# Optimization experiments

Hardware: AMD Instinct MI355X
Metric: run time of the kernel (lower is better)

## Reference

```python
import jax, jax.numpy as jnp
import numpy as np

N_NODES = 50000
N_EDGES = 800000
IN_DIM = 128
EDGE_DIM = 32
HID = 64


def _glorot(key, shape):
    fan_in, fan_out = shape[0], shape[1]
    lim = float(np.sqrt(6.0 / (fan_in + fan_out)))
    return jax.random.uniform(key, shape, jnp.float32, -lim, lim)


def setup_inputs() -> dict:
    key = jax.random.key(0)
    ks = jax.random.split(key, 16)
    x = jax.random.normal(ks[0], (N_NODES, IN_DIM), jnp.float32)
    edge_index = jax.random.randint(ks[1], (2, N_EDGES), 0, N_NODES, jnp.int64)
    edge_attr = jax.random.normal(ks[2], (N_EDGES, EDGE_DIM), jnp.float32)
    message = jax.random.normal(ks[3], (N_EDGES, HID), jnp.float32)
    return {
        "x": x,
        "edge_index": edge_index,
        "edge_attr": edge_attr,
        "message": message,
        "W_src": _glorot(ks[4], (IN_DIM, HID)),
        "W_dest": _glorot(ks[5], (IN_DIM, HID)),
        "W_edge": _glorot(ks[6], (EDGE_DIM, HID)),
        "attn_vec": _glorot(ks[7], (1, HID)),
        "mlp_w1": _glorot(ks[8], (2 * HID, HID)),
        "mlp_b1": jnp.zeros((HID,), jnp.float32),
        "bn1_g": jnp.ones((HID,), jnp.float32),
        "bn1_b": jnp.zeros((HID,), jnp.float32),
        "mlp_w2": _glorot(ks[9], (HID, HID)),
        "mlp_b2": jnp.zeros((HID,), jnp.float32),
        "bn2_g": jnp.ones((HID,), jnp.float32),
        "bn2_b": jnp.zeros((HID,), jnp.float32),
        "amlp_w": _glorot(ks[10], (HID, 1)),
        "amlp_b": jnp.zeros((1,), jnp.float32),
    }


def _batchnorm(h, g, b, eps=1e-5):
    mu = jnp.mean(h, axis=0)
    var = jnp.var(h, axis=0)  # biased, as torch BN training forward
    return (h - mu) * jax.lax.rsqrt(var + eps) * g + b


def _segment_softmax(scores, seg, num_segments):
    m = jax.ops.segment_max(scores, seg, num_segments=num_segments)
    m = jnp.where(jnp.isneginf(m), 0.0, m)
    e = jnp.exp(scores - m[seg])
    s = jax.ops.segment_sum(e, seg, num_segments=num_segments)
    return e / s[seg]


def _scatter_max0(vals, seg, num_segments):
    # torch_scatter reduce='max' fills empty segments with 0
    out = jax.ops.segment_max(vals, seg, num_segments=num_segments)
    return jnp.where(jnp.isneginf(out), 0.0, out)


def reference(x, edge_index, edge_attr, message, W_src, W_dest, W_edge, attn_vec,
              mlp_w1, mlp_b1, bn1_g, bn1_b, mlp_w2, mlp_b2, bn2_g, bn2_b,
              amlp_w, amlp_b):
    row, col = edge_index[0], edge_index[1]
    # attention scores per edge
    h = x[row] @ W_src + x[col] @ W_dest + edge_attr @ W_edge  # [E, H]
    scores = jax.nn.leaky_relu(h @ attn_vec[0], negative_slope=0.2)  # [E]
    attn = _segment_softmax(scores, col, N_NODES)  # [E]
    msg = message * attn[:, None]  # [E, H]
    fwd = _scatter_max0(msg, col, N_NODES)  # [N, H]
    bwd = _scatter_max0(msg, row, N_NODES)  # [N, H]
    out = jnp.concatenate([fwd, bwd], axis=1)  # [N, 2H]
    # node MLP (BatchNorm in training-stats mode, dropout disabled)
    h1 = jax.nn.relu(_batchnorm(out @ mlp_w1 + mlp_b1, bn1_g, bn1_b))
    h2 = jax.nn.relu(_batchnorm(h1 @ mlp_w2 + mlp_b2, bn2_g, bn2_b))
    gate = jax.nn.sigmoid(h2 @ amlp_w + amlp_b).reshape(-1)  # [N]
    return h2, gate
```

## Files before the change

### kernel.cpp

```cpp
#include <hip/hip_runtime.h>
#include <hip/hip_bf16.h>
#include <float.h>

#define IN_DIM 128
#define EDGE_DIM 32
#define HID 64
#define BKT_G 64
#define BCAP 3072
#define NBKT_MAX 784
#define CHUNK 4096

__global__ void k_uvw(const float* __restrict__ Wsrc, const float* __restrict__ Wdst,
                      const float* __restrict__ Wedge, const float* __restrict__ avec,
                      const int* __restrict__ ei32, int* sflag,
                      float* u, float* v, float* w) {
    if (blockIdx.x == 0 && threadIdx.x == 0) {
        int odd_or = ei32[1] | ei32[3] | ei32[5] | ei32[7] | ei32[9] | ei32[11];
        sflag[0] = (odd_or == 0) ? 2 : 1;
    }
    int wave = (blockIdx.x * blockDim.x + threadIdx.x) >> 6;
    int lane = threadIdx.x & 63;
    const float* src; float* dst; int row;
    if (wave < 128)      { src = Wsrc;  dst = u; row = wave; }
    else if (wave < 256) { src = Wdst;  dst = v; row = wave - 128; }
    else if (wave < 288) { src = Wedge; dst = w; row = wave - 256; }
    else return;
    float acc = src[row * HID + lane] * avec[lane];
    for (int o = 32; o >= 1; o >>= 1) acc += __shfl_xor(acc, o);
    if (lane == 0) dst[row] = acc;
}

__global__ void k_pq(const float* __restrict__ x, const float* __restrict__ u,
                     const float* __restrict__ v, float* p, float* q, int N) {
    int wave = (blockIdx.x * blockDim.x + threadIdx.x) >> 6;
    int lane = threadIdx.x & 63;
    if (wave >= N) return;
    const float* xr = x + (size_t)wave * IN_DIM;
    float a0 = xr[lane], a1 = xr[lane + 64];
    float pp = a0 * u[lane] + a1 * u[lane + 64];
    float qq = a0 * v[lane] + a1 * v[lane + 64];
    for (int m = 32; m >= 1; m >>= 1) { pp += __shfl_xor(pp, m); qq += __shfl_xor(qq, m); }
    if (lane == 0) { p[wave] = pp; q[wave] = qq; }
}

__global__ void k_edot(const float* __restrict__ ea, const float* __restrict__ w,
                       float* rdot, int E) {
    int gid = blockIdx.x * blockDim.x + threadIdx.x;
    int e = gid >> 3;
    int j = gid & 7;
    if (e >= E) return;
    float4 av = ((const float4*)ea)[(size_t)e * 8 + j];
    float4 wv = ((const float4*)w)[j];
    float val = av.x * wv.x + av.y * wv.y + av.z * wv.z + av.w * wv.w;
    val += __shfl_xor(val, 4);
    val += __shfl_xor(val, 2);
    val += __shfl_xor(val, 1);
    if (j == 0) rdot[e] = val;
}

__global__ __launch_bounds__(256) void k_binscore(const int* __restrict__ ei,
                                                  const int* __restrict__ sflag,
                                                  const float* __restrict__ rdot,
                                                  const float* __restrict__ p,
                                                  const float* __restrict__ q,
                                                  float* scores,
                                                  int* gcur_col, int* gcur_row,
                                                  unsigned* bbuf_col, unsigned* bbuf_row,
                                                  int E, int nbkt) {
    __shared__ int lc[NBKT_MAX], lrw[NBKT_MAX];
    __shared__ int gc[NBKT_MAX], grw[NBKT_MAX];
    int tid = threadIdx.x;
    int e0 = blockIdx.x * CHUNK;
    int e1 = e0 + CHUNK; if (e1 > E) e1 = E;
    for (int i = tid; i < nbkt; i += 256) { lc[i] = 0; lrw[i] = 0; }
    __syncthreads();
    int st = sflag[0];
    for (int e = e0 + tid; e < e1; e += 256) {
        int r = ei[(size_t)st * e];
        int c = ei[(size_t)st * (E + e)];
        float sc = rdot[e] + p[r] + q[c];
        scores[e] = (sc > 0.f) ? sc : 0.2f * sc;
        atomicAdd(&lc[c >> 6], 1);
        atomicAdd(&lrw[r >> 6], 1);
    }
    __syncthreads();
    for (int b = tid; b < nbkt; b += 256) {
        int n1 = lc[b];  if (n1) gc[b]  = atomicAdd(&gcur_col[b], n1);
        int n2 = lrw[b]; if (n2) grw[b] = atomicAdd(&gcur_row[b], n2);
        lc[b] = 0; lrw[b] = 0;
    }
    __syncthreads();
    for (int e = e0 + tid; e < e1; e += 256) {
        int r = ei[(size_t)st * e];
        int c = ei[(size_t)st * (E + e)];
        int pos = gc[c >> 6] + atomicAdd(&lc[c >> 6], 1);
        if (pos < BCAP) bbuf_col[(size_t)(c >> 6) * BCAP + pos] = (unsigned)((e << 6) | (c & 63));
        int pos2 = grw[r >> 6] + atomicAdd(&lrw[r >> 6], 1);
        if (pos2 < BCAP) bbuf_row[(size_t)(r >> 6) * BCAP + pos2] = (unsigned)((e << 6) | (r & 63));
    }
}

__global__ __launch_bounds__(512) void k_sortfwd(float* scores, const float* __restrict__ msg,
                                                 const int* __restrict__ bcur,
                                                 const unsigned* __restrict__ bbuf,
                                                 float* fwd, int N) {
    __shared__ unsigned raw[BCAP];
    __shared__ unsigned srt[BCAP];
    __shared__ float    ssc[BCAP];
    __shared__ int cnt[BKT_G], cur[BKT_G], sstart[BKT_G + 1];
    int b = blockIdx.x, tid = threadIdx.x;
    int M = bcur[b]; if (M > BCAP) M = BCAP;
    if (tid < BKT_G) cnt[tid] = 0;
    __syncthreads();
    for (int i = tid; i < M; i += 512) {
        unsigned v = bbuf[(size_t)b * BCAP + i];
        raw[i] = v;
        atomicAdd(&cnt[v & 63], 1);
    }
    __syncthreads();
    if (tid < BKT_G) {
        int val = cnt[tid];
        int inc = val;
        for (int off = 1; off < BKT_G; off <<= 1) {
            int o = __shfl_up(inc, off);
            if (tid >= off) inc += o;
        }
        sstart[tid + 1] = inc;
        if (tid == 0) sstart[0] = 0;
        cur[tid] = inc - val;
    }
    __syncthreads();
    for (int j = tid; j < M; j += 512) {
        unsigned v = raw[j];
        int posn = atomicAdd(&cur[v & 63], 1);
        srt[posn] = v;
    }
    __syncthreads();
    for (int i = tid; i < M; i += 512) ssc[i] = scores[srt[i] >> 6];
    __syncthreads();
    int wave = tid >> 6, lane = tid & 63;
    for (int n = wave; n < BKT_G; n += 8) {
        int node = b * BKT_G + n;
        if (node >= N) continue;
        int a0 = sstart[n], len = sstart[n + 1] - a0;
        if (len == 0) { fwd[(size_t)node * HID + lane] = 0.f; continue; }
        float m = -FLT_MAX;
        for (int k = lane; k < len; k += 64) m = fmaxf(m, ssc[a0 + k]);
        for (int o = 32; o >= 1; o >>= 1) m = fmaxf(m, __shfl_xor(m, o));
        float ssum = 0.f;
        for (int k = lane; k < len; k += 64) ssum += expf(ssc[a0 + k] - m);
        for (int o = 32; o >= 1; o >>= 1) ssum += __shfl_xor(ssum, o);
        float rcp = 1.f / ssum;
        for (int k = lane; k < len; k += 64) {
            int i = a0 + k;
            float at = expf(ssc[i] - m) * rcp;
            ssc[i] = at;
            scores[srt[i] >> 6] = at;
        }
        asm volatile("s_waitcnt lgkmcnt(0)" ::: "memory");
        float acc = -FLT_MAX;
        int k = 0;
        for (; k + 8 <= len; k += 8) {
            float vv[8];
#pragma unroll
            for (int u8 = 0; u8 < 8; u8++) {
                int i = a0 + k + u8;
                vv[u8] = msg[(size_t)(srt[i] >> 6) * HID + lane] * ssc[i];
            }
#pragma unroll
            for (int u8 = 0; u8 < 8; u8++) acc = fmaxf(acc, vv[u8]);
        }
        for (; k < len; k++) {
            int i = a0 + k;
            acc = fmaxf(acc, msg[(size_t)(srt[i] >> 6) * HID + lane] * ssc[i]);
        }
        fwd[(size_t)node * HID + lane] = acc;
    }
}

__global__ __launch_bounds__(512) void k_sortbwd(const float* __restrict__ scores,
                                                 const float* __restrict__ msg,
                                                 const int* __restrict__ bcur,
                                                 const unsigned* __restrict__ bbuf,
                                                 float* bwd, int N) {
    __shared__ unsigned raw[BCAP];
    __shared__ unsigned srt[BCAP];
    __shared__ float    ssc[BCAP];
    __shared__ int cnt[BKT_G], cur[BKT_G], sstart[BKT_G + 1];
    int b = blockIdx.x, tid = threadIdx.x;
    int M = bcur[b]; if (M > BCAP) M = BCAP;
    if (tid < BKT_G) cnt[tid] = 0;
    __syncthreads();
    for (int i = tid; i < M; i += 512) {
        unsigned v = bbuf[(size_t)b * BCAP + i];
        raw[i] = v;
        atomicAdd(&cnt[v & 63], 1);
    }
    __syncthreads();
    if (tid < BKT_G) {
        int val = cnt[tid];
        int inc = val;
        for (int off = 1; off < BKT_G; off <<= 1) {
            int o = __shfl_up(inc, off);
            if (tid >= off) inc += o;
        }
        sstart[tid + 1] = inc;
        if (tid == 0) sstart[0] = 0;
        cur[tid] = inc - val;
    }
    __syncthreads();
    for (int j = tid; j < M; j += 512) {
        unsigned v = raw[j];
        int posn = atomicAdd(&cur[v & 63], 1);
        srt[posn] = v;
    }
    __syncthreads();
    for (int i = tid; i < M; i += 512) ssc[i] = scores[srt[i] >> 6];
    __syncthreads();
    int wave = tid >> 6, lane = tid & 63;
    for (int n = wave; n < BKT_G; n += 8) {
        int node = b * BKT_G + n;
        if (node >= N) continue;
        int a0 = sstart[n], len = sstart[n + 1] - a0;
        if (len == 0) { bwd[(size_t)node * HID + lane] = 0.f; continue; }
        float acc = -FLT_MAX;
        int k = 0;
        for (; k + 8 <= len; k += 8) {
            float vv[8];
#pragma unroll
            for (int u8 = 0; u8 < 8; u8++) {
                int i = a0 + k + u8;
                vv[u8] = msg[(size_t)(srt[i] >> 6) * HID + lane] * ssc[i];
            }
#pragma unroll
            for (int u8 = 0; u8 < 8; u8++) acc = fmaxf(acc, vv[u8]);
        }
        for (; k < len; k++) {
            int i = a0 + k;
            acc = fmaxf(acc, msg[(size_t)(srt[i] >> 6) * HID + lane] * ssc[i]);
        }
        bwd[(size_t)node * HID + lane] = acc;
    }
}

__global__ __launch_bounds__(256) void k_mlp1(const float* __restrict__ fwd,
                                              const float* __restrict__ bwd,
                                              const float* __restrict__ W1,
                                              const float* __restrict__ b1,
                                              float* pre1, float* gsum, float* gss, int N) {
    __shared__ float lsum[HID], lss[HID];
    int t = threadIdx.x;
    if (t < HID) { lsum[t] = 0.f; lss[t] = 0.f; }
    __syncthreads();
    int h = t & 63, lr = t >> 6;
    float bh = b1[h];
    float s = 0.f, ssq = 0.f;
    for (int n = blockIdx.x * 4 + lr; n < N; n += gridDim.x * 4) {
        const float* fr = fwd + (size_t)n * HID;
        const float* br = bwd + (size_t)n * HID;
        float acc = bh;
        for (int k = 0; k < HID; k++) acc += fr[k] * W1[k * HID + h];
        for (int k = 0; k < HID; k++) acc += br[k] * W1[(HID + k) * HID + h];
        pre1[(size_t)n * HID + h] = acc;
        s += acc; ssq += acc * acc;
    }
    atomicAdd(&lsum[h], s);
    atomicAdd(&lss[h], ssq);
    __syncthreads();
    if (t < HID) { atomicAdd(&gsum[t], lsum[t]); atomicAdd(&gss[t], lss[t]); }
}

__global__ void k_bnfin(const float* __restrict__ gsum, const float* __restrict__ gss,
                        const float* __restrict__ g, const float* __restrict__ b,
                        float* scale, float* shift, int N) {
    int t = threadIdx.x;
    if (t >= HID) return;
    float invN = 1.0f / (float)N;
    float mu = gsum[t] * invN;
    float var = gss[t] * invN - mu * mu;
    float rs = rsqrtf(var + 1e-5f);
    float sc = rs * g[t];
    scale[t] = sc;
    shift[t] = b[t] - mu * sc;
}

__global__ __launch_bounds__(256) void k_mlp2(const float* __restrict__ pre1,
                                              const float* __restrict__ scale1,
                                              const float* __restrict__ shift1,
                                              const float* __restrict__ W2,
                                              const float* __restrict__ b2v,
                                              float* pre2, float* gsum, float* gss, int N) {
    __shared__ float lsum[HID], lss[HID];
    int t = threadIdx.x;
    if (t < HID) { lsum[t] = 0.f; lss[t] = 0.f; }
    __syncthreads();
    int h = t & 63, lr = t >> 6;
    float bh = b2v[h];
    float s = 0.f, ssq = 0.f;
    for (int n = blockIdx.x * 4 + lr; n < N; n += gridDim.x * 4) {
        const float* pr = pre1 + (size_t)n * HID;
        float acc = bh;
        for (int k = 0; k < HID; k++) {
            float z = pr[k] * scale1[k] + shift1[k];
            z = (z > 0.f) ? z : 0.f;
            acc += z * W2[k * HID + h];
        }
        pre2[(size_t)n * HID + h] = acc;
        s += acc; ssq += acc * acc;
    }
    atomicAdd(&lsum[h], s);
    atomicAdd(&lss[h], ssq);
    __syncthreads();
    if (t < HID) { atomicAdd(&gsum[t], lsum[t]); atomicAdd(&gss[t], lss[t]); }
}

__global__ void k_out(const float* __restrict__ pre2, const float* __restrict__ scale2,
                      const float* __restrict__ shift2, const float* __restrict__ amw,
                      const float* __restrict__ amb, float* out, int N) {
    int gid = blockIdx.x * blockDim.x + threadIdx.x;
    int n = gid >> 6, h = gid & 63;
    if (n >= N) return;
    float z = pre2[(size_t)n * HID + h] * scale2[h] + shift2[h];
    float h2 = (z > 0.f) ? z : 0.f;
    out[(size_t)n * HID + h] = h2;
    float part = h2 * amw[h];
    for (int m = 32; m >= 1; m >>= 1) part += __shfl_xor(part, m);
    if (h == 0) {
        float gate = 1.0f / (1.0f + expf(-(part + amb[0])));
        out[(size_t)N * HID + n] = gate;
    }
}

extern "C" void kernel_launch(void* const* d_in, const int* in_sizes, int n_in,
                              void* d_out, int out_size, void* d_ws, size_t ws_size,
                              hipStream_t stream) {
    const float* x     = (const float*)d_in[0];
    const int*   ei    = (const int*)d_in[1];
    const float* ea    = (const float*)d_in[2];
    const float* msg   = (const float*)d_in[3];
    const float* Wsrc  = (const float*)d_in[4];
    const float* Wdst  = (const float*)d_in[5];
    const float* Wedge = (const float*)d_in[6];
    const float* avec  = (const float*)d_in[7];
    const float* W1    = (const float*)d_in[8];
    const float* b1    = (const float*)d_in[9];
    const float* g1    = (const float*)d_in[10];
    const float* bb1   = (const float*)d_in[11];
    const float* W2    = (const float*)d_in[12];
    const float* b2    = (const float*)d_in[13];
    const float* g2    = (const float*)d_in[14];
    const float* bb2   = (const float*)d_in[15];
    const float* amw   = (const float*)d_in[16];
    const float* amb   = (const float*)d_in[17];
    float* out = (float*)d_out;

    const int N = in_sizes[0] / IN_DIM;
    const int E = in_sizes[1] / 2;
    const int NH = N * HID;
    const int nbkt = (N + BKT_G - 1) / BKT_G;

    float* ws = (float*)d_ws;
    float* gsum1  = ws;
    float* gss1   = ws + 64;
    float* gsum2  = ws + 128;
    float* gss2   = ws + 192;
    float* scale1 = ws + 256;
    float* shift1 = ws + 320;
    float* scale2 = ws + 384;
    float* shift2 = ws + 448;
    int*   sflag  = (int*)(ws + 512);
    float* u      = ws + 576;
    float* v      = ws + 704;
    float* w      = ws + 832;
    float* T        = ws + 1024;
    float* p        = T;
    float* q        = p + N;
    float* scores   = q + N;
    float* rdot     = scores + E;
    int*   gcur_col = (int*)(rdot + E);
    int*   gcur_row = gcur_col + nbkt;
    unsigned* bbuf_col = (unsigned*)(gcur_row + nbkt);
    unsigned* bbuf_row = bbuf_col + (size_t)nbkt * BCAP;
    size_t T_words  = 2 * (size_t)N + 2 * (size_t)E + 2 * (size_t)nbkt
                    + 2 * (size_t)nbkt * BCAP;
    size_t T_sz     = (T_words < (size_t)NH) ? (size_t)NH : T_words;
    float* fwd  = ws + 1024 + T_sz;
    float* bwd  = fwd + (size_t)NH;
    float* pre1 = T;
    float* pre2 = fwd;

    (void)hipMemsetAsync(gcur_col, 0, (size_t)2 * nbkt * sizeof(int), stream);
    (void)hipMemsetAsync(ws, 0, 512 * sizeof(float), stream);
    hipLaunchKernelGGL(k_uvw, dim3(72), dim3(256), 0, stream,
                       Wsrc, Wdst, Wedge, avec, ei, sflag, u, v, w);
    hipLaunchKernelGGL(k_pq, dim3((N * 64 + 255) / 256), dim3(256), 0, stream,
                       x, u, v, p, q, N);
    hipLaunchKernelGGL(k_edot, dim3((E * 8 + 255) / 256), dim3(256), 0, stream,
                       ea, w, rdot, E);
    hipLaunchKernelGGL(k_binscore, dim3((E + CHUNK - 1) / CHUNK), dim3(256), 0, stream,
                       ei, sflag, rdot, p, q, scores,
                       gcur_col, gcur_row, bbuf_col, bbuf_row, E, nbkt);
    hipLaunchKernelGGL(k_sortfwd, dim3(nbkt), dim3(512), 0, stream,
                       scores, msg, gcur_col, bbuf_col, fwd, N);
    hipLaunchKernelGGL(k_sortbwd, dim3(nbkt), dim3(512), 0, stream,
                       scores, msg, gcur_row, bbuf_row, bwd, N);
    hipLaunchKernelGGL(k_mlp1, dim3(1024), dim3(256), 0, stream,
                       fwd, bwd, W1, b1, pre1, gsum1, gss1, N);
    hipLaunchKernelGGL(k_bnfin, dim3(1), dim3(64), 0, stream,
                       gsum1, gss1, g1, bb1, scale1, shift1, N);
    hipLaunchKernelGGL(k_mlp2, dim3(1024), dim3(256), 0, stream,
                       pre1, scale1, shift1, W2, b2, pre2, gsum2, gss2, N);
    hipLaunchKernelGGL(k_bnfin, dim3(1), dim3(64), 0, stream,
                       gsum2, gss2, g2, bb2, scale2, shift2, N);
    hipLaunchKernelGGL(k_out, dim3((N * 64 + 255) / 256), dim3(256), 0, stream,
                       pre2, scale2, shift2, amw, amb, out, N);
}
```

Baseline: 372.2 us.

## Fuse node MLP, batchnorm and gate into one cooperative kernel with grid sync

Replaces the five node-MLP launches (mlp1, bnfin, mlp2, bnfin, out) with a single cooperative kernel. Each wave keeps its per-row pre-activations in registers across two grid-wide syncs, and batchnorm statistics are reduced through global atomics. This removes launch overhead and the global round trips for pre1 and pre2. It adds grid.sync cost, depends on all 1024 blocks being co-resident, and falls back to the old launch path if the cooperative launch fails.

```diff
diff --git a/kernel.cpp b/kernel.cpp
--- a/kernel.cpp
+++ b/kernel.cpp
@@ -1,6 +1,9 @@
 #include <hip/hip_runtime.h>
 #include <hip/hip_bf16.h>
+#include <hip/hip_cooperative_groups.h>
 #include <float.h>
+
+namespace cg = cooperative_groups;
 
 #define IN_DIM 128
 #define EDGE_DIM 32
@@ -9,6 +12,8 @@
 #define BCAP 3072
 #define NBKT_MAX 784
 #define CHUNK 4096
+#define MLP_GRID 1024
+#define ROWS_MAX 13
 
 __global__ void k_uvw(const float* __restrict__ Wsrc, const float* __restrict__ Wdst,
                       const float* __restrict__ Wedge, const float* __restrict__ avec,
@@ -243,6 +248,108 @@
     }
 }
 
+__global__ __launch_bounds__(256, 4) void k_mlpfused(
+        const float* __restrict__ fwd, const float* __restrict__ bwd,
+        const float* __restrict__ W1, const float* __restrict__ b1,
+        const float* __restrict__ g1, const float* __restrict__ bb1,
+        const float* __restrict__ W2, const float* __restrict__ b2,
+        const float* __restrict__ g2, const float* __restrict__ bb2,
+        const float* __restrict__ amw, const float* __restrict__ amb,
+        float* gstats, float* out, int N) {
+    cg::grid_group grid = cg::this_grid();
+    __shared__ float lsum[HID], lss[HID];
+    __shared__ float sscale[HID], sshift[HID];
+    const int t = threadIdx.x, h = t & 63, lr = t >> 6;
+    const int nwave = MLP_GRID * 4;
+    const int wgid = blockIdx.x * 4 + lr;
+    float pre1r[ROWS_MAX], pre2r[ROWS_MAX];
+    const float invN = 1.0f / (float)N;
+
+    if (t < HID) { lsum[t] = 0.f; lss[t] = 0.f; }
+    __syncthreads();
+    float bh = b1[h];
+    float s = 0.f, ssq = 0.f;
+#pragma unroll
+    for (int i = 0; i < ROWS_MAX; i++) {
+        int n = wgid + i * nwave;
+        if (n < N) {
+            const float* fr = fwd + (size_t)n * HID;
+            const float* br = bwd + (size_t)n * HID;
+            float acc = bh;
+            for (int k = 0; k < HID; k++) acc += fr[k] * W1[k * HID + h];
+            for (int k = 0; k < HID; k++) acc += br[k] * W1[(HID + k) * HID + h];
+            pre1r[i] = acc;
+            s += acc; ssq += acc * acc;
+        } else pre1r[i] = 0.f;
+    }
+    atomicAdd(&lsum[h], s);
+    atomicAdd(&lss[h], ssq);
+    __syncthreads();
+    if (t < HID) { atomicAdd(&gstats[t], lsum[t]); atomicAdd(&gstats[HID + t], lss[t]); }
+    grid.sync();
+
+    if (t < HID) {
+        float gs = atomicAdd(&gstats[t], 0.0f);
+        float gq = atomicAdd(&gstats[HID + t], 0.0f);
+        float mu = gs * invN;
+        float var = gq * invN - mu * mu;
+        float rs = rsqrtf(var + 1e-5f);
+        float sc = rs * g1[t];
+        sscale[t] = sc;
+        sshift[t] = bb1[t] - mu * sc;
+        lsum[t] = 0.f; lss[t] = 0.f;
+    }
+    __syncthreads();
+
+    float b2h = b2[h];
+    s = 0.f; ssq = 0.f;
+#pragma unroll
+    for (int i = 0; i < ROWS_MAX; i++) {
+        int n = wgid + i * nwave;
+        float z = pre1r[i] * sscale[h] + sshift[h];
+        z = (z > 0.f) ? z : 0.f;
+        float acc = b2h;
+        for (int k = 0; k < HID; k++) {
+            float zk = __shfl(z, k);
+            acc += zk * W2[k * HID + h];
+        }
+        if (n < N) { pre2r[i] = acc; s += acc; ssq += acc * acc; }
+        else pre2r[i] = 0.f;
+    }
+    atomicAdd(&lsum[h], s);
+    atomicAdd(&lss[h], ssq);
+    __syncthreads();
+    if (t < HID) { atomicAdd(&gstats[2 * HID + t], lsum[t]); atomicAdd(&gstats[3 * HID + t], lss[t]); }
+    grid.sync();
+
+    if (t < HID) {
+        float gs = atomicAdd(&gstats[2 * HID + t], 0.0f);
+        float gq = atomicAdd(&gstats[3 * HID + t], 0.0f);
+        float mu = gs * invN;
+        float var = gq * invN - mu * mu;
+        float rs = rsqrtf(var + 1e-5f);
+        float sc = rs * g2[t];
+        sscale[t] = sc;
+        sshift[t] = bb2[t] - mu * sc;
+    }
+    __syncthreads();
+    float aw = amw[h], ab = amb[0];
+#pragma unroll
+    for (int i = 0; i < ROWS_MAX; i++) {
+        int n = wgid + i * nwave;
+        if (n >= N) continue;
+        float z = pre2r[i] * sscale[h] + sshift[h];
+        float h2 = (z > 0.f) ? z : 0.f;
+        out[(size_t)n * HID + h] = h2;
+        float part = h2 * aw;
+        for (int m = 32; m >= 1; m >>= 1) part += __shfl_xor(part, m);
+        if (h == 0) {
+            float gate = 1.0f / (1.0f + expf(-(part + ab)));
+            out[(size_t)N * HID + n] = gate;
+        }
+    }
+}
+
 __global__ __launch_bounds__(256) void k_mlp1(const float* __restrict__ fwd,
                                               const float* __restrict__ bwd,
                                               const float* __restrict__ W1,
@@ -342,16 +449,16 @@
     const float* Wdst  = (const float*)d_in[5];
     const float* Wedge = (const float*)d_in[6];
     const float* avec  = (const float*)d_in[7];
-    const float* W1    = (const float*)d_in[8];
-    const float* b1    = (const float*)d_in[9];
-    const float* g1    = (const float*)d_in[10];
-    const float* bb1   = (const float*)d_in[11];
-    const float* W2    = (const float*)d_in[12];
-    const float* b2    = (const float*)d_in[13];
-    const float* g2    = (const float*)d_in[14];
-    const float* bb2   = (const float*)d_in[15];
-    const float* amw   = (const float*)d_in[16];
-    const float* amb   = (const float*)d_in[17];
+    const float* W1  = (const float*)d_in[8];
+    const float* b1  = (const float*)d_in[9];
+    const float* g1  = (const float*)d_in[10];
+    const float* bb1 = (const float*)d_in[11];
+    const float* W2  = (const float*)d_in[12];
+    const float* b2  = (const float*)d_in[13];
+    const float* g2  = (const float*)d_in[14];
+    const float* bb2 = (const float*)d_in[15];
+    const float* amw = (const float*)d_in[16];
+    const float* amb = (const float*)d_in[17];
     float* out = (float*)d_out;
 
     const int N = in_sizes[0] / IN_DIM;
@@ -360,6 +467,7 @@
     const int nbkt = (N + BKT_G - 1) / BKT_G;
 
     float* ws = (float*)d_ws;
+    float* gstats = ws;
     float* gsum1  = ws;
     float* gss1   = ws + 64;
     float* gsum2  = ws + 128;
@@ -404,14 +512,24 @@
                        scores, msg, gcur_col, bbuf_col, fwd, N);
     hipLaunchKernelGGL(k_sortbwd, dim3(nbkt), dim3(512), 0, stream,
                        scores, msg, gcur_row, bbuf_row, bwd, N);
-    hipLaunchKernelGGL(k_mlp1, dim3(1024), dim3(256), 0, stream,
-                       fwd, bwd, W1, b1, pre1, gsum1, gss1, N);
-    hipLaunchKernelGGL(k_bnfin, dim3(1), dim3(64), 0, stream,
-                       gsum1, gss1, g1, bb1, scale1, shift1, N);
-    hipLaunchKernelGGL(k_mlp2, dim3(1024), dim3(256), 0, stream,
-                       pre1, scale1, shift1, W2, b2, pre2, gsum2, gss2, N);
-    hipLaunchKernelGGL(k_bnfin, dim3(1), dim3(64), 0, stream,
-                       gsum2, gss2, g2, bb2, scale2, shift2, N);
-    hipLaunchKernelGGL(k_out, dim3((N * 64 + 255) / 256), dim3(256), 0, stream,
-                       pre2, scale2, shift2, amw, amb, out, N);
-}
+
+    void* args[] = { (void*)&fwd, (void*)&bwd, (void*)&W1, (void*)&b1,
+                     (void*)&g1, (void*)&bb1, (void*)&W2, (void*)&b2,
+                     (void*)&g2, (void*)&bb2, (void*)&amw, (void*)&amb,
+                     (void*)&gstats, (void*)&out, (void*)&N };
+    hipError_t cerr = hipLaunchCooperativeKernel((const void*)k_mlpfused,
+                                                 dim3(MLP_GRID), dim3(256),
+                                                 args, 0, stream);
+    if (cerr != hipSuccess) {
+        hipLaunchKernelGGL(k_mlp1, dim3(1024), dim3(256), 0, stream,
+                           fwd, bwd, W1, b1, pre1, gsum1, gss1, N);
+        hipLaunchKernelGGL(k_bnfin, dim3(1), dim3(64), 0, stream,
+                           gsum1, gss1, g1, bb1, scale1, shift1, N);
+        hipLaunchKernelGGL(k_mlp2, dim3(1024), dim3(256), 0, stream,
+                           pre1, scale1, shift1, W2, b2, pre2, gsum2, gss2, N);
+        hipLaunchKernelGGL(k_bnfin, dim3(1), dim3(64), 0, stream,
+                           gsum2, gss2, g2, bb2, scale2, shift2, N);
+        hipLaunchKernelGGL(k_out, dim3((N * 64 + 255) / 256), dim3(256), 0, stream,
+                           pre2, scale2, shift2, amw, amb, out, N);
+    }
+}
```

Measured after the change: 617.3 us. +65.9%, slower.
